# Kernel tuning notes

Measured on AMD Instinct MI355X. Metric: run time of the kernel, lower is better.

## Reference

```python
import jax, jax.numpy as jnp
import numpy as np

# Dims (match init_kwargs)
B, N, D_MODEL = 64, 64, 512
D_STATE = 512
D_ATT = D_MODEL
H, W, C, K = 128, 128, 16, 5
T = 32  # num_steps
HALF = K // 2


def _lin(key, out_d, in_d):
    kw, kb = jax.random.split(key)
    w = jax.random.normal(kw, (out_d, in_d), jnp.float32) * 0.02
    b = jax.random.normal(kb, (out_d,), jnp.float32) * 0.02
    return w, b


def setup_inputs() -> dict:
    key = jax.random.key(0)
    ks = jax.random.split(key, 12)
    token_reps = jax.random.normal(ks[0], (B, N, D_MODEL), jnp.float32)
    global_rep = jax.random.normal(ks[1], (B, D_MODEL), jnp.float32)
    attention_mask = jnp.ones((B, N), jnp.int32)
    w_init, b_init = _lin(ks[2], D_STATE, D_MODEL)
    wq, bq = _lin(ks[3], D_ATT, D_STATE)
    wk, bk = _lin(ks[4], D_ATT, D_MODEL)
    wv, bv = _lin(ks[5], D_ATT, D_MODEL)
    gru_in = D_ATT + D_MODEL
    w_ih, b_ih = _lin(ks[6], 3 * D_STATE, gru_in)
    w_hh, b_hh = _lin(ks[7], 3 * D_STATE, D_STATE)
    w_write, b_write = _lin(ks[8], C * K * K, D_STATE + D_ATT)
    w_loc, b_loc = _lin(ks[9], 3, D_STATE + D_ATT + D_MODEL)
    return dict(token_reps=token_reps, global_rep=global_rep, attention_mask=attention_mask,
                w_init=w_init, b_init=b_init, wq=wq, bq=bq, wk=wk, bk=bk, wv=wv, bv=bv,
                w_ih=w_ih, b_ih=b_ih, w_hh=w_hh, b_hh=b_hh,
                w_write=w_write, b_write=b_write, w_loc=w_loc, b_loc=b_loc)


def _forward(token_reps, global_rep, attention_mask,
             w_init, b_init, wq, bq, wk, bk, wv, bv,
             w_ih, b_ih, w_hh, b_hh, w_write, b_write, w_loc, b_loc):
    Bv = token_reps.shape[0]
    # Precompute keys/values (constant over steps)
    k_tok = token_reps @ wk.T + bk  # [B,N,d_att]
    v_tok = token_reps @ wv.T + bv  # [B,N,d_att]
    invalid = attention_mask == 0

    s0 = jnp.tanh(global_rep @ w_init.T + b_init)  # [B,d_state]
    # Padded canvas (NHWC): full KxK patches always fit; crop at the end
    # reproduces the torch clipped-window write exactly.
    canvas0 = jnp.zeros((Bv, H + 2 * HALF, W + 2 * HALF, C), jnp.float32)
    b_idx = jnp.arange(Bv)
    koff = jnp.arange(K)

    def step(carry, _):
        s, canvas_p = carry
        q = s @ wq.T + bq  # [B,d_att]
        scores = jnp.einsum('bd,bnd->bn', q, k_tok)
        scores = jnp.where(invalid, -1e9, scores)
        alpha = jax.nn.softmax(scores, axis=-1)
        r = jnp.einsum('bn,bnd->bd', alpha, v_tok)  # [B,d_att]
        # GRUCell (torch gate order r,z,n)
        x = jnp.concatenate([r, global_rep], axis=-1)
        gi = x @ w_ih.T + b_ih
        gh = s @ w_hh.T + b_hh
        ir, iz, inn = jnp.split(gi, 3, axis=-1)
        hr, hz, hn = jnp.split(gh, 3, axis=-1)
        rg = jax.nn.sigmoid(ir + hr)
        zg = jax.nn.sigmoid(iz + hz)
        ng = jnp.tanh(inn + rg * hn)
        s_new = (1.0 - zg) * ng + zg * s
        # Write patch
        patch = (jnp.concatenate([s_new, r], axis=-1) @ w_write.T + b_write)
        patch = patch.reshape(Bv, C, K, K).transpose(0, 2, 3, 1)  # [B,K,K,C]
        loc = jnp.concatenate([s_new, r, global_rep], axis=-1) @ w_loc.T + b_loc
        cx = jnp.tanh(loc[:, 0])
        cy = jnp.tanh(loc[:, 1])
        j = jnp.clip(jnp.round(0.5 * (cx + 1.0) * (W - 1)), 0, W - 1).astype(jnp.int32)
        i = jnp.clip(jnp.round(0.5 * (cy + 1.0) * (H - 1)), 0, H - 1).astype(jnp.int32)
        # padded coords: top-left of window in padded canvas is (i, j)
        rows = i[:, None] + koff  # [B,K]
        cols = j[:, None] + koff  # [B,K]
        canvas_p = canvas_p.at[b_idx[:, None, None], rows[:, :, None], cols[:, None, :]].add(patch)
        return (s_new, canvas_p), None

    (_, canvas_p), _ = jax.lax.scan(step, (s0, canvas0), None, length=T)
    canvas = canvas_p[:, HALF:HALF + H, HALF:HALF + W, :].transpose(0, 3, 1, 2)  # [B,C,H,W]
    return canvas


def reference(token_reps, global_rep, attention_mask,
              w_init, b_init, wq, bq, wk, bk, wv, bv,
              w_ih, b_ih, w_hh, b_hh, w_write, b_write, w_loc, b_loc):
    return _forward(token_reps, global_rep, attention_mask,
                    w_init, b_init, wq, bq, wk, bk, wv, bv,
                    w_ih, b_ih, w_hh, b_hh, w_write, b_write, w_loc, b_loc)
```

## Files before the change

### kernel.cpp

```cpp
#include <hip/hip_runtime.h>

#define BB 64
#define DD 512
#define TT 32

__device__ __forceinline__ float dot4(const float4 a, const float4 b) {
  return a.x * b.x + a.y * b.y + a.z * b.z + a.w * b.w;
}

__device__ __forceinline__ void cst(float* p, float v) {
  __hip_atomic_store(p, v, __ATOMIC_RELAXED, __HIP_MEMORY_SCOPE_AGENT);
}

__global__ void zero_k(float* __restrict__ out, int n4) {
  const int i = blockIdx.x * blockDim.x + threadIdx.x;
  if (i < n4) ((float4*)out)[i] = make_float4(0.f, 0.f, 0.f, 0.f);
}

__global__ void vecs_k(const float* __restrict__ wq, const float* __restrict__ bk,
                       const float* __restrict__ wk, const float* __restrict__ bq,
                       float* __restrict__ kqb, float* __restrict__ wkbq,
                       float* __restrict__ bqbk, unsigned* __restrict__ bar) {
  const int tid = threadIdx.x, bz = blockIdx.x;
  if (bz < 2) {
    const int d = bz * 256 + tid;
    float s = 0.f;
    for (int e = 0; e < DD; ++e) s += wq[e * DD + d] * bk[e];
    kqb[d] = s;
  } else {
    const int k = (bz - 2) * 256 + tid;
    float s = 0.f;
    for (int e = 0; e < DD; ++e) s += bq[e] * wk[e * DD + k];
    wkbq[k] = s;
    if (bz == 2 && tid == 0) {
      float t2 = 0.f;
      for (int e = 0; e < DD; ++e) t2 += bq[e] * bk[e];
      *bqbk = t2;
    }
    if (bz == 3) {
      if (tid < 16)
        __hip_atomic_store(bar + tid * 64, 0u, __ATOMIC_RELAXED, __HIP_MEMORY_SCOPE_AGENT);
      __hip_atomic_store(bar + 1024 + tid * 32, 0u, __ATOMIC_RELAXED, __HIP_MEMORY_SCOPE_AGENT);
    }
  }
}

__global__ __launch_bounds__(256) void gemm128_k(
    const float* __restrict__ A, int lda, int a_trans,
    const float* __restrict__ B, int ldb, int boff, int b_trans,
    const float* __restrict__ bias, float* __restrict__ C, long c_stride_z, int ldc,
    int kfrom, int klen, int act) {
  __shared__ __align__(16) float As[16][132];
  __shared__ __align__(16) float Bs[16][68];
  const int tid = threadIdx.x;
  const int tx = tid & 15, ty = tid >> 4;
  const int m0 = blockIdx.x * 128, n0 = blockIdx.y * 64;
  const int kbase = kfrom + blockIdx.z * klen;
  float* Ce = C + (long)blockIdx.z * c_stride_z;
  float acc[8][4];
#pragma unroll
  for (int i = 0; i < 8; ++i)
#pragma unroll
    for (int j = 0; j < 4; ++j) acc[i][j] = 0.f;

  for (int k0 = kbase; k0 < kbase + klen; k0 += 16) {
    if (!a_trans) {
      const int row = tid >> 1, half = tid & 1;
      const float* ap = A + (long)(m0 + row) * lda + k0 + half * 8;
      const float4 a0 = *(const float4*)ap;
      const float4 a1 = *(const float4*)(ap + 4);
      const int kb = half * 8;
      As[kb + 0][row] = a0.x; As[kb + 1][row] = a0.y; As[kb + 2][row] = a0.z; As[kb + 3][row] = a0.w;
      As[kb + 4][row] = a1.x; As[kb + 5][row] = a1.y; As[kb + 6][row] = a1.z; As[kb + 7][row] = a1.w;
    } else {
      const int kk = tid >> 4, mseg = tid & 15;
      const float* ap = A + (long)(k0 + kk) * lda + m0 + mseg * 8;
      *(float4*)&As[kk][mseg * 8] = *(const float4*)ap;
      *(float4*)&As[kk][mseg * 8 + 4] = *(const float4*)(ap + 4);
    }
    if (!b_trans) {
      const int n = tid >> 2, q = tid & 3;
      const float4 b0 = *(const float4*)(B + (long)(n0 + n) * ldb + boff + k0 + q * 4);
      Bs[q * 4 + 0][n] = b0.x; Bs[q * 4 + 1][n] = b0.y; Bs[q * 4 + 2][n] = b0.z; Bs[q * 4 + 3][n] = b0.w;
    } else {
      const int kk = tid >> 4, nq = tid & 15;
      *(float4*)&Bs[kk][nq * 4] = *(const float4*)(B + (long)(k0 + kk) * ldb + boff + n0 + nq * 4);
    }
    __syncthreads();
#pragma unroll
    for (int kk = 0; kk < 16; ++kk) {
      const float4 a0 = *(const float4*)&As[kk][ty * 8];
      const float4 a1 = *(const float4*)&As[kk][ty * 8 + 4];
      const float4 b0 = *(const float4*)&Bs[kk][tx * 4];
      const float am[8] = {a0.x, a0.y, a0.z, a0.w, a1.x, a1.y, a1.z, a1.w};
#pragma unroll
      for (int i = 0; i < 8; ++i) {
        acc[i][0] += am[i] * b0.x; acc[i][1] += am[i] * b0.y;
        acc[i][2] += am[i] * b0.z; acc[i][3] += am[i] * b0.w;
      }
    }
    __syncthreads();
  }
  float4 bv = make_float4(0.f, 0.f, 0.f, 0.f);
  if (bias) bv = *(const float4*)(bias + n0 + tx * 4);
#pragma unroll
  for (int i = 0; i < 8; ++i) {
    const int m = m0 + ty * 8 + i;
    float4 v = make_float4(acc[i][0] + bv.x, acc[i][1] + bv.y, acc[i][2] + bv.z, acc[i][3] + bv.w);
    if (act == 1) { v.x = tanhf(v.x); v.y = tanhf(v.y); v.z = tanhf(v.z); v.w = tanhf(v.w); }
    *(float4*)&Ce[(long)m * ldc + n0 + tx * 4] = v;
  }
}

__global__ __launch_bounds__(256) void gemm128_dual_k(
    const float* __restrict__ A,
    const float* __restrict__ B0, const float* __restrict__ bias0, float* __restrict__ C0,
    const float* __restrict__ B1, const float* __restrict__ bias1, float* __restrict__ C1) {
  __shared__ __align__(16) float As[16][132];
  __shared__ __align__(16) float Bs[16][68];
  const int tid = threadIdx.x;
  const int tx = tid & 15, ty = tid >> 4;
  const int m0 = blockIdx.x * 128, n0 = blockIdx.y * 64;
  const float* B = blockIdx.z ? B1 : B0;
  const float* bias = blockIdx.z ? bias1 : bias0;
  float* C = blockIdx.z ? C1 : C0;
  float acc[8][4];
#pragma unroll
  for (int i = 0; i < 8; ++i)
#pragma unroll
    for (int j = 0; j < 4; ++j) acc[i][j] = 0.f;

  for (int k0 = 0; k0 < 512; k0 += 16) {
    {
      const int row = tid >> 1, half = tid & 1;
      const float* ap = A + (long)(m0 + row) * 512 + k0 + half * 8;
      const float4 a0 = *(const float4*)ap;
      const float4 a1 = *(const float4*)(ap + 4);
      const int kb = half * 8;
      As[kb + 0][row] = a0.x; As[kb + 1][row] = a0.y; As[kb + 2][row] = a0.z; As[kb + 3][row] = a0.w;
      As[kb + 4][row] = a1.x; As[kb + 5][row] = a1.y; As[kb + 6][row] = a1.z; As[kb + 7][row] = a1.w;
    }
    {
      const int n = tid >> 2, q = tid & 3;
      const float4 b0 = *(const float4*)(B + (long)(n0 + n) * 512 + k0 + q * 4);
      Bs[q * 4 + 0][n] = b0.x; Bs[q * 4 + 1][n] = b0.y; Bs[q * 4 + 2][n] = b0.z; Bs[q * 4 + 3][n] = b0.w;
    }
    __syncthreads();
#pragma unroll
    for (int kk = 0; kk < 16; ++kk) {
      const float4 a0 = *(const float4*)&As[kk][ty * 8];
      const float4 a1 = *(const float4*)&As[kk][ty * 8 + 4];
      const float4 b0 = *(const float4*)&Bs[kk][tx * 4];
      const float am[8] = {a0.x, a0.y, a0.z, a0.w, a1.x, a1.y, a1.z, a1.w};
#pragma unroll
      for (int i = 0; i < 8; ++i) {
        acc[i][0] += am[i] * b0.x; acc[i][1] += am[i] * b0.y;
        acc[i][2] += am[i] * b0.z; acc[i][3] += am[i] * b0.w;
      }
    }
    __syncthreads();
  }
  const float4 bvv = *(const float4*)(bias + n0 + tx * 4);
#pragma unroll
  for (int i = 0; i < 8; ++i) {
    const int m = m0 + ty * 8 + i;
    float4 v = make_float4(acc[i][0] + bvv.x, acc[i][1] + bvv.y, acc[i][2] + bvv.z, acc[i][3] + bvv.w);
    *(float4*)&C[(long)m * 512 + n0 + tx * 4] = v;
  }
}

__global__ void combine4_k(const float* __restrict__ p, float* __restrict__ out) {
  const int i = blockIdx.x * blockDim.x + threadIdx.x;
  const float4 a = ((const float4*)p)[i];
  const float4 b = ((const float4*)p)[i + 65536];
  const float4 c = ((const float4*)p)[i + 131072];
  const float4 d = ((const float4*)p)[i + 196608];
  ((float4*)out)[i] = make_float4(a.x + b.x + c.x + d.x, a.y + b.y + c.y + d.y,
                                  a.z + b.z + c.z + d.z, a.w + b.w + c.w + d.w);
}

__global__ __launch_bounds__(256) void gemm_k(
    const float* __restrict__ A, int lda, int a_trans,
    const float* __restrict__ B, int ldb, int boff, int b_trans,
    const float* __restrict__ bias,
    float* __restrict__ C, int ldc, int M, int N, int K, int act) {
  __shared__ __align__(16) float As2[32][68];
  __shared__ __align__(16) float Bs2[32][68];
  const int tid = threadIdx.x;
  const int tx = tid & 15, ty = tid >> 4;
  const int m0 = blockIdx.x * 64, n0 = blockIdx.y * 64;
  float acc[4][4] = {};
  for (int k0 = 0; k0 < K; k0 += 32) {
    {
      const int r = tid >> 2, cg2 = (tid & 3) * 8;
      const float* ap = A + (long)(m0 + r) * lda + k0 + cg2;
      const float4 a0 = *(const float4*)ap;
      const float4 a1 = *(const float4*)(ap + 4);
      As2[cg2 + 0][r] = a0.x; As2[cg2 + 1][r] = a0.y; As2[cg2 + 2][r] = a0.z; As2[cg2 + 3][r] = a0.w;
      As2[cg2 + 4][r] = a1.x; As2[cg2 + 5][r] = a1.y; As2[cg2 + 6][r] = a1.z; As2[cg2 + 7][r] = a1.w;
    }
    {
      const int r = tid >> 2, cg2 = (tid & 3) * 8;
      float4 b0 = make_float4(0.f, 0.f, 0.f, 0.f);
      float4 b1 = make_float4(0.f, 0.f, 0.f, 0.f);
      if (n0 + r < N) {
        const float* bp = B + (long)(n0 + r) * ldb + boff + k0 + cg2;
        b0 = *(const float4*)bp;
        b1 = *(const float4*)(bp + 4);
      }
      Bs2[cg2 + 0][r] = b0.x; Bs2[cg2 + 1][r] = b0.y; Bs2[cg2 + 2][r] = b0.z; Bs2[cg2 + 3][r] = b0.w;
      Bs2[cg2 + 4][r] = b1.x; Bs2[cg2 + 5][r] = b1.y; Bs2[cg2 + 6][r] = b1.z; Bs2[cg2 + 7][r] = b1.w;
    }
    __syncthreads();
#pragma unroll
    for (int kk = 0; kk < 32; ++kk) {
      const float4 av = *(const float4*)&As2[kk][ty * 4];
      const float4 bv = *(const float4*)&Bs2[kk][tx * 4];
      acc[0][0] += av.x * bv.x; acc[0][1] += av.x * bv.y; acc[0][2] += av.x * bv.z; acc[0][3] += av.x * bv.w;
      acc[1][0] += av.y * bv.x; acc[1][1] += av.y * bv.y; acc[1][2] += av.y * bv.z; acc[1][3] += av.y * bv.w;
      acc[2][0] += av.z * bv.x; acc[2][1] += av.z * bv.y; acc[2][2] += av.z * bv.z; acc[2][3] += av.z * bv.w;
      acc[3][0] += av.w * bv.x; acc[3][1] += av.w * bv.y; acc[3][2] += av.w * bv.z; acc[3][3] += av.w * bv.w;
    }
    __syncthreads();
  }
#pragma unroll
  for (int i = 0; i < 4; ++i) {
    const int m = m0 + ty * 4 + i;
#pragma unroll
    for (int j = 0; j < 4; ++j) {
      const int n = n0 + tx * 4 + j;
      if (n < N) {
        float v = acc[i][j] + (bias ? bias[n] : 0.f);
        if (act == 1) v = tanhf(v);
        C[(long)m * ldc + n] = v;
      }
    }
  }
}

__device__ __forceinline__ void grid_barrier(unsigned* __restrict__ bar, unsigned gen) {
  __syncthreads();
  const int blk = blockIdx.x, tid = threadIdx.x;
  unsigned* gctr = bar;
  unsigned* rel = bar + 1024;
  if (blk == 0) {
    if (tid == 0)
      __hip_atomic_fetch_add(gctr, 1u, __ATOMIC_RELAXED, __HIP_MEMORY_SCOPE_AGENT);
    if (tid < 16) {
      while (__hip_atomic_load(gctr + tid * 64, __ATOMIC_RELAXED, __HIP_MEMORY_SCOPE_AGENT) < gen * 16u)
        __builtin_amdgcn_s_sleep(1);
    }
    __syncthreads();
    __hip_atomic_store(rel + tid * 32, gen, __ATOMIC_RELAXED, __HIP_MEMORY_SCOPE_AGENT);
  } else {
    if (tid == 0) {
      __hip_atomic_fetch_add(gctr + (blk >> 4) * 64, 1u, __ATOMIC_RELAXED, __HIP_MEMORY_SCOPE_AGENT);
      while (__hip_atomic_load(rel + blk * 32, __ATOMIC_RELAXED, __HIP_MEMORY_SCOPE_AGENT) < gen)
        __builtin_amdgcn_s_sleep(1);
    }
  }
  __syncthreads();
}

__global__ __launch_bounds__(256, 1) void loop_k(
    const float* __restrict__ ktil, const float* __restrict__ cbn,
    const float* __restrict__ vt, const float* __restrict__ locg,
    float* __restrict__ sbuf, float* __restrict__ rbuf,
    const float* __restrict__ w_write, const float* __restrict__ b_write,
    const float* __restrict__ w_loc, const int* __restrict__ amask,
    float* __restrict__ canvas, const float* __restrict__ gig,
    const float* __restrict__ w_ih, const float* __restrict__ w_hh,
    const float* __restrict__ b_hh, unsigned* __restrict__ bar) {
  __shared__ __align__(16) float smem[10048];
  __shared__ __align__(16) float wpl[12288];
  float* sm_act = smem;
  float* sm_val = smem + 9216;
  float* sm_sc  = smem + 9408;
  float* sm_s   = smem;
  float* sm_r   = smem + 4608;
  float* sm_g   = smem + 9216;

  const int blk = blockIdx.x, tid = threadIdx.x, lane = tid & 63;
  const bool is_attn = (blk < 64);
  const bool is_patch = (blk >= 64) && (blk < 224);
  unsigned nsync = 0;

  int p_rg = 0, p_bg = 0;
  if (is_patch) {
    const int g = blk - 64;
    p_bg = g & 3; p_rg = g >> 2;
    for (int idx = tid; idx < 3072; idx += 256) {
      const int rho = idx >> 8, f4 = idx & 255;
      const int col = f4 << 2;
      const int cc = col >> 5, jj = (col >> 2) & 7;
      const int dcol = (cc << 5) | ((jj ^ (cc & 7)) << 2);
      const float* src = (rho < 10) ? (w_write + (long)(p_rg * 10 + rho) * 1024 + col)
                                    : (w_loc + (long)(rho - 10) * 1536 + col);
      *(float4*)(wpl + rho * 1024 + dcol) = *(const float4*)src;
    }
  }

  float4 wg[3][8];
  const int g_dg = blk & 63, g_bg = blk >> 6;
  {
    const int c = tid & 15, sl = tid >> 4;
#pragma unroll
    for (int i = 0; i < 3; ++i) {
      const int rho = sl * 3 + i;
      const float* wsrc;
      if (rho < 24) {
        const int g2 = rho >> 3, di = rho & 7;
        wsrc = w_ih + (long)(g2 * 512 + g_dg * 8 + di) * 1024 + c * 32;
      } else {
        const int rh = rho - 24, g2 = rh >> 3, di = rh & 7;
        wsrc = w_hh + (long)(g2 * 512 + g_dg * 8 + di) * 512 + c * 32;
      }
#pragma unroll
      for (int j = 0; j < 8; ++j) wg[i][j] = *(const float4*)(wsrc + 4 * j);
    }
  }
  __syncthreads();

  for (int t = 0; t <= TT; ++t) {
    const float* s_cur = sbuf + (long)t * (BB * DD);
    float* r_cur = rbuf + (long)t * (BB * DD);
    const float* r_prev = r_cur - BB * DD;

    if (is_attn) {
      if (t < TT) {
        const int b = blk, wrp = tid >> 6;
        const float* sb = s_cur + (long)b * DD;
        const float4 sva = *(const float4*)(sb + lane * 8);
        const float4 svb = *(const float4*)(sb + lane * 8 + 4);
        for (int h8 = 0; h8 < 2; ++h8) {
          const float* kbase = ktil + ((long)(b * 64 + wrp * 16 + h8 * 8)) * DD + lane * 8;
          float4 ka[8], kb2[8];
#pragma unroll
          for (int i = 0; i < 8; ++i) {
            ka[i] = *(const float4*)(kbase + (long)i * DD);
            kb2[i] = *(const float4*)(kbase + (long)i * DD + 4);
          }
#pragma unroll
          for (int i = 0; i < 8; ++i) {
            float p = dot4(ka[i], sva) + dot4(kb2[i], svb);
#pragma unroll
            for (int off = 32; off; off >>= 1) p += __shfl_xor(p, off);
            if (lane == 0) {
              const int n = wrp * 16 + h8 * 8 + i;
              float sc = p + cbn[b * 64 + n];
              if (amask[b * 64 + n] == 0) sc = -1e9f;
              sm_sc[n] = sc;
            }
          }
        }
        __syncthreads();
        if (tid < 64) {
          const float v = sm_sc[tid];
          float m = v;
#pragma unroll
          for (int off = 32; off; off >>= 1) m = fmaxf(m, __shfl_xor(m, off));
          const float e = expf(v - m);
          float l2 = e;
#pragma unroll
          for (int off = 32; off; off >>= 1) l2 += __shfl_xor(l2, off);
          sm_sc[tid] = e / l2;
        }
        __syncthreads();
        float rx = 0.f, ry = 0.f;
        const float* vb = vt + (long)b * 64 * DD + (tid << 1);
        for (int n0 = 0; n0 < 64; n0 += 8) {
          float2 vv[8];
#pragma unroll
          for (int i = 0; i < 8; ++i)
            vv[i] = *(const float2*)(vb + (long)(n0 + i) * DD);
#pragma unroll
          for (int i = 0; i < 8; ++i) {
            const float a = sm_sc[n0 + i];
            rx = fmaf(a, vv[i].x, rx);
            ry = fmaf(a, vv[i].y, ry);
          }
        }
        cst(r_cur + b * DD + (tid << 1), rx);
        cst(r_cur + b * DD + (tid << 1) + 1, ry);
      }
    } else if (is_patch) {
      if (t >= 1) {
        const int c = tid & 31, sl = tid >> 5;
        const int tr = sl & 3, bgsub = sl >> 2;
        for (int h = 0; h < 2; ++h) {
          __syncthreads();
          {
            const int b_i8 = tid >> 5, l = tid & 31;
            const int b = p_bg * 16 + h * 8 + b_i8;
            const float* sp = s_cur + (long)b * DD + l * 16;
            const float* rp = r_prev + (long)b * DD + l * 16;
            float* dsd = sm_act + b_i8 * 1152 + (l >> 1) * 36 + (l & 1) * 16;
            float* drd = sm_act + b_i8 * 1152 + (16 + (l >> 1)) * 36 + (l & 1) * 16;
#pragma unroll
            for (int jj = 0; jj < 4; ++jj) {
              *(float4*)(dsd + 4 * jj) = *(const float4*)(sp + 4 * jj);
              *(float4*)(drd + 4 * jj) = *(const float4*)(rp + 4 * jj);
            }
          }
          __syncthreads();
          float4 wreg[3][8];
#pragma unroll
          for (int i = 0; i < 3; ++i) {
            const float* wrow = wpl + (tr * 3 + i) * 1024 + (c << 5);
#pragma unroll
            for (int j = 0; j < 8; ++j)
              wreg[i][j] = *(const float4*)(wrow + ((j ^ (c & 7)) << 2));
          }
          for (int bi = 0; bi < 4; ++bi) {
            const int bl = bgsub * 4 + bi;
            const int babs = p_bg * 16 + h * 8 + bl;
            const float* ap = sm_act + bl * 1152 + c * 36;
            float a0 = 0.f, a1 = 0.f, a2 = 0.f;
#pragma unroll
            for (int j = 0; j < 8; ++j) {
              const float4 av = *(const float4*)(ap + 4 * j);
              a0 += dot4(wreg[0][j], av);
              a1 += dot4(wreg[1][j], av);
              a2 += dot4(wreg[2][j], av);
            }
#pragma unroll
            for (int m = 1; m < 32; m <<= 1) {
              a0 += __shfl_xor(a0, m);
              a1 += __shfl_xor(a1, m);
              a2 += __shfl_xor(a2, m);
            }
            if (c == 0) {
              const int bslot = h * 8 + bl;
              const float av3[3] = {a0, a1, a2};
#pragma unroll
              for (int i = 0; i < 3; ++i) {
                const int rho = tr * 3 + i;
                float v = av3[i];
                if (rho >= 10) v += locg[babs * 2 + (rho - 10)];
                sm_val[rho * 16 + bslot] = v;
              }
            }
          }
        }
        __syncthreads();
        if (tid < 160) {
          const int ri = tid >> 4, bl2 = tid & 15;
          const int row = p_rg * 10 + ri;
          const int b = p_bg * 16 + bl2;
          const float val = sm_val[ri * 16 + bl2] + b_write[row];
          const float lx = sm_val[10 * 16 + bl2];
          const float ly = sm_val[11 * 16 + bl2];
          const int jx = min(127, max(0, (int)rintf(0.5f * (tanhf(lx) + 1.f) * 127.f)));
          const int iy = min(127, max(0, (int)rintf(0.5f * (tanhf(ly) + 1.f) * 127.f)));
          const int cc = row / 25, rem = row % 25, ki = rem / 5, kj = rem % 5;
          const int y = iy + ki - 2, x = jx + kj - 2;
          if (y >= 0 && y < 128 && x >= 0 && x < 128)
            atomicAdd(canvas + ((((long)b * 16 + cc) * 128 + y) * 128 + x), val);
        }
      }
    }

    if (t == TT) break;

    grid_barrier(bar, ++nsync);

    {
      float* s_nxt = sbuf + (long)(t + 1) * (BB * DD);
      const int c = tid & 15, sl = tid >> 4;
      for (int h = 0; h < 2; ++h) {
        __syncthreads();
        {
          const int b_i8 = tid >> 5, l = tid & 31;
          const int b = g_bg * 16 + h * 8 + b_i8;
          const float* sp = s_cur + (long)b * DD + l * 16;
          const float* rp = r_cur + (long)b * DD + l * 16;
          float* dsd = sm_s + b_i8 * 576 + (l >> 1) * 36 + (l & 1) * 16;
          float* drd = sm_r + b_i8 * 576 + (l >> 1) * 36 + (l & 1) * 16;
#pragma unroll
          for (int jj = 0; jj < 4; ++jj) {
            *(float4*)(dsd + 4 * jj) = *(const float4*)(sp + 4 * jj);
            *(float4*)(drd + 4 * jj) = *(const float4*)(rp + 4 * jj);
          }
        }
        __syncthreads();
        const float* base = (sl < 8) ? sm_r : sm_s;
        for (int bl = 0; bl < 8; ++bl) {
          const float* ap = base + bl * 576 + c * 36;
          float a0 = 0.f, a1 = 0.f, a2 = 0.f;
#pragma unroll
          for (int j = 0; j < 8; ++j) {
            const float4 av = *(const float4*)(ap + 4 * j);
            a0 += dot4(wg[0][j], av);
            a1 += dot4(wg[1][j], av);
            a2 += dot4(wg[2][j], av);
          }
#pragma unroll
          for (int m = 1; m < 16; m <<= 1) {
            a0 += __shfl_xor(a0, m);
            a1 += __shfl_xor(a1, m);
            a2 += __shfl_xor(a2, m);
          }
          if (c == 0) {
            const int bslot = h * 8 + bl;
            sm_g[bslot * 52 + sl * 3 + 0] = a0;
            sm_g[bslot * 52 + sl * 3 + 1] = a1;
            sm_g[bslot * 52 + sl * 3 + 2] = a2;
          }
        }
      }
      __syncthreads();
      if (tid < 128) {
        const int b_i = tid >> 3, di = tid & 7;
        const int b = g_bg * 16 + b_i, d = g_dg * 8 + di;
        const float ir = sm_g[b_i * 52 + di]        + gig[b * 1536 + d];
        const float iz = sm_g[b_i * 52 + 8 + di]    + gig[b * 1536 + 512 + d];
        const float in = sm_g[b_i * 52 + 16 + di]   + gig[b * 1536 + 1024 + d];
        const float hr = sm_g[b_i * 52 + 24 + di]   + b_hh[d];
        const float hz = sm_g[b_i * 52 + 32 + di]   + b_hh[512 + d];
        const float hn = sm_g[b_i * 52 + 40 + di]   + b_hh[1024 + d];
        const float rg2 = 1.f / (1.f + expf(-(ir + hr)));
        const float zg = 1.f / (1.f + expf(-(iz + hz)));
        const float ng = tanhf(in + rg2 * hn);
        const float sprev = s_cur[(long)b * DD + d];
        cst(s_nxt + (long)b * DD + d, (1.f - zg) * ng + zg * sprev);
      }
    }

    grid_barrier(bar, ++nsync);
  }
}

extern "C" void kernel_launch(void* const* d_in, const int* in_sizes, int n_in,
                              void* d_out, int out_size, void* d_ws, size_t ws_size,
                              hipStream_t stream) {
  const float* tok     = (const float*)d_in[0];
  const float* grep    = (const float*)d_in[1];
  const int*   amask   = (const int*)d_in[2];
  const float* w_init  = (const float*)d_in[3];
  const float* b_init  = (const float*)d_in[4];
  const float* wq      = (const float*)d_in[5];
  const float* bq      = (const float*)d_in[6];
  const float* wk      = (const float*)d_in[7];
  const float* bk      = (const float*)d_in[8];
  const float* wv      = (const float*)d_in[9];
  const float* bv      = (const float*)d_in[10];
  const float* w_ih    = (const float*)d_in[11];
  const float* b_ih    = (const float*)d_in[12];
  const float* w_hh    = (const float*)d_in[13];
  const float* b_hh    = (const float*)d_in[14];
  const float* w_write = (const float*)d_in[15];
  const float* b_write = (const float*)d_in[16];
  const float* w_loc   = (const float*)d_in[17];
  const float* b_loc   = (const float*)d_in[18];
  float* canvas = (float*)d_out;

  float* ws = (float*)d_ws;
  float* ktil = ws;
  float* vtw  = ktil + 2097152;
  float* Aqk  = vtw + 2097152;
  float* gig  = Aqk + 262144;
  float* cbn  = gig + 98304;
  float* sbuf = cbn + 4096;
  float* rbuf = sbuf + 1081344;
  float* locg = rbuf + 1048576;
  float* kqb  = locg + 128;
  float* wkbq = kqb + 512;
  float* bqbk = wkbq + 512;
  unsigned* bar = (unsigned*)(bqbk + 64);

  zero_k<<<16384, 256, 0, stream>>>(canvas, 16777216 / 4);
  vecs_k<<<4, 256, 0, stream>>>(wq, bk, wk, bq, kqb, wkbq, bqbk, bar);
  gemm128_k<<<dim3(4, 8, 4), 256, 0, stream>>>(wq, 512, 1, wk, 512, 0, 1,
                                               nullptr, vtw, 262144L, 512, 0, 128, 0);
  combine4_k<<<256, 256, 0, stream>>>(vtw, Aqk);
  gemm128_dual_k<<<dim3(32, 8, 2), 256, 0, stream>>>(tok, Aqk, kqb, ktil, wv, bv, vtw);
  gemm_k<<<dim3(64, 1), 256, 0, stream>>>(tok, 512, 0, wkbq, 0, 0, 0, bqbk, cbn, 1, 4096, 1, 512, 0);
  gemm_k<<<dim3(1, 24), 256, 0, stream>>>(grep, 512, 0, w_ih, 1024, 512, 0, b_ih, gig, 1536, 64, 1536, 512, 0);
  gemm_k<<<dim3(1, 8), 256, 0, stream>>>(grep, 512, 0, w_init, 512, 0, 0, b_init, sbuf, 512, 64, 512, 512, 1);
  gemm_k<<<dim3(1, 1), 256, 0, stream>>>(grep, 512, 0, w_loc, 1536, 1024, 0, b_loc, locg, 2, 64, 2, 512, 0);

  loop_k<<<256, 256, 0, stream>>>(ktil, cbn, vtw, locg, sbuf, rbuf, w_write, b_write,
                                  w_loc, amask, canvas, gig, w_ih, w_hh, b_hh, bar);
}
```

Measured before the change: 1.134 ms.

## Decouple patch blocks from grid barrier and defer canvas writes to separate kernel

```diff
diff --git a/kernel.cpp b/kernel.cpp
--- a/kernel.cpp
+++ b/kernel.cpp
@@ -10,11 +10,6 @@
 
 __device__ __forceinline__ void cst(float* p, float v) {
   __hip_atomic_store(p, v, __ATOMIC_RELAXED, __HIP_MEMORY_SCOPE_AGENT);
-}
-
-__global__ void zero_k(float* __restrict__ out, int n4) {
-  const int i = blockIdx.x * blockDim.x + threadIdx.x;
-  if (i < n4) ((float4*)out)[i] = make_float4(0.f, 0.f, 0.f, 0.f);
 }
 
 __global__ void vecs_k(const float* __restrict__ wq, const float* __restrict__ bk,
@@ -238,7 +233,7 @@
   }
 }
 
-__device__ __forceinline__ void grid_barrier(unsigned* __restrict__ bar, unsigned gen) {
+__device__ __forceinline__ void ag_barrier(unsigned* __restrict__ bar, unsigned gen) {
   __syncthreads();
   const int blk = blockIdx.x, tid = threadIdx.x;
   unsigned* gctr = bar;
@@ -246,12 +241,13 @@
   if (blk == 0) {
     if (tid == 0)
       __hip_atomic_fetch_add(gctr, 1u, __ATOMIC_RELAXED, __HIP_MEMORY_SCOPE_AGENT);
-    if (tid < 16) {
+    if (tid < 4) {
       while (__hip_atomic_load(gctr + tid * 64, __ATOMIC_RELAXED, __HIP_MEMORY_SCOPE_AGENT) < gen * 16u)
         __builtin_amdgcn_s_sleep(1);
     }
     __syncthreads();
-    __hip_atomic_store(rel + tid * 32, gen, __ATOMIC_RELAXED, __HIP_MEMORY_SCOPE_AGENT);
+    if (tid < 224)
+      __hip_atomic_store(rel + tid * 32, gen, __ATOMIC_RELAXED, __HIP_MEMORY_SCOPE_AGENT);
   } else {
     if (tid == 0) {
       __hip_atomic_fetch_add(gctr + (blk >> 4) * 64, 1u, __ATOMIC_RELAXED, __HIP_MEMORY_SCOPE_AGENT);
@@ -268,214 +264,51 @@
     float* __restrict__ sbuf, float* __restrict__ rbuf,
     const float* __restrict__ w_write, const float* __restrict__ b_write,
     const float* __restrict__ w_loc, const int* __restrict__ amask,
-    float* __restrict__ canvas, const float* __restrict__ gig,
-    const float* __restrict__ w_ih, const float* __restrict__ w_hh,
-    const float* __restrict__ b_hh, unsigned* __restrict__ bar) {
-  __shared__ __align__(16) float smem[10048];
-  __shared__ __align__(16) float wpl[12288];
-  float* sm_act = smem;
-  float* sm_val = smem + 9216;
-  float* sm_sc  = smem + 9408;
-  float* sm_s   = smem;
-  float* sm_r   = smem + 4608;
-  float* sm_g   = smem + 9216;
-
+    float* __restrict__ patchbuf, float* __restrict__ locbuf,
+    const float* __restrict__ gig, const float* __restrict__ w_ih,
+    const float* __restrict__ w_hh, const float* __restrict__ b_hh,
+    unsigned* __restrict__ bar) {
+  __shared__ __align__(16) float smem[38272];
   const int blk = blockIdx.x, tid = threadIdx.x, lane = tid & 63;
-  const bool is_attn = (blk < 64);
-  const bool is_patch = (blk >= 64) && (blk < 224);
-  unsigned nsync = 0;
-
-  int p_rg = 0, p_bg = 0;
-  if (is_patch) {
+  unsigned* rel = bar + 1024;
+
+  if (blk >= 64) {
+    float* wpl    = smem;
+    float* sm_act = smem + 12288;
+    float* sm_val = smem + 21504;
     const int g = blk - 64;
-    p_bg = g & 3; p_rg = g >> 2;
+    const int p_bg = g & 3, p_rg = g >> 2;
     for (int idx = tid; idx < 3072; idx += 256) {
       const int rho = idx >> 8, f4 = idx & 255;
       const int col = f4 << 2;
-      const int cc = col >> 5, jj = (col >> 2) & 7;
-      const int dcol = (cc << 5) | ((jj ^ (cc & 7)) << 2);
+      const int cc2 = col >> 5, jj = (col >> 2) & 7;
+      const int dcol = (cc2 << 5) | ((jj ^ (cc2 & 7)) << 2);
       const float* src = (rho < 10) ? (w_write + (long)(p_rg * 10 + rho) * 1024 + col)
                                     : (w_loc + (long)(rho - 10) * 1536 + col);
       *(float4*)(wpl + rho * 1024 + dcol) = *(const float4*)src;
     }
-  }
-
-  float4 wg[3][8];
-  const int g_dg = blk & 63, g_bg = blk >> 6;
-  {
-    const int c = tid & 15, sl = tid >> 4;
-#pragma unroll
-    for (int i = 0; i < 3; ++i) {
-      const int rho = sl * 3 + i;
-      const float* wsrc;
-      if (rho < 24) {
-        const int g2 = rho >> 3, di = rho & 7;
-        wsrc = w_ih + (long)(g2 * 512 + g_dg * 8 + di) * 1024 + c * 32;
-      } else {
-        const int rh = rho - 24, g2 = rh >> 3, di = rh & 7;
-        wsrc = w_hh + (long)(g2 * 512 + g_dg * 8 + di) * 512 + c * 32;
-      }
-#pragma unroll
-      for (int j = 0; j < 8; ++j) wg[i][j] = *(const float4*)(wsrc + 4 * j);
-    }
-  }
-  __syncthreads();
-
-  for (int t = 0; t <= TT; ++t) {
-    const float* s_cur = sbuf + (long)t * (BB * DD);
-    float* r_cur = rbuf + (long)t * (BB * DD);
-    const float* r_prev = r_cur - BB * DD;
-
-    if (is_attn) {
-      if (t < TT) {
-        const int b = blk, wrp = tid >> 6;
-        const float* sb = s_cur + (long)b * DD;
-        const float4 sva = *(const float4*)(sb + lane * 8);
-        const float4 svb = *(const float4*)(sb + lane * 8 + 4);
-        for (int h8 = 0; h8 < 2; ++h8) {
-          const float* kbase = ktil + ((long)(b * 64 + wrp * 16 + h8 * 8)) * DD + lane * 8;
-          float4 ka[8], kb2[8];
-#pragma unroll
-          for (int i = 0; i < 8; ++i) {
-            ka[i] = *(const float4*)(kbase + (long)i * DD);
-            kb2[i] = *(const float4*)(kbase + (long)i * DD + 4);
-          }
-#pragma unroll
-          for (int i = 0; i < 8; ++i) {
-            float p = dot4(ka[i], sva) + dot4(kb2[i], svb);
-#pragma unroll
-            for (int off = 32; off; off >>= 1) p += __shfl_xor(p, off);
-            if (lane == 0) {
-              const int n = wrp * 16 + h8 * 8 + i;
-              float sc = p + cbn[b * 64 + n];
-              if (amask[b * 64 + n] == 0) sc = -1e9f;
-              sm_sc[n] = sc;
-            }
-          }
-        }
-        __syncthreads();
-        if (tid < 64) {
-          const float v = sm_sc[tid];
-          float m = v;
-#pragma unroll
-          for (int off = 32; off; off >>= 1) m = fmaxf(m, __shfl_xor(m, off));
-          const float e = expf(v - m);
-          float l2 = e;
-#pragma unroll
-          for (int off = 32; off; off >>= 1) l2 += __shfl_xor(l2, off);
-          sm_sc[tid] = e / l2;
-        }
-        __syncthreads();
-        float rx = 0.f, ry = 0.f;
-        const float* vb = vt + (long)b * 64 * DD + (tid << 1);
-        for (int n0 = 0; n0 < 64; n0 += 8) {
-          float2 vv[8];
-#pragma unroll
-          for (int i = 0; i < 8; ++i)
-            vv[i] = *(const float2*)(vb + (long)(n0 + i) * DD);
-#pragma unroll
-          for (int i = 0; i < 8; ++i) {
-            const float a = sm_sc[n0 + i];
-            rx = fmaf(a, vv[i].x, rx);
-            ry = fmaf(a, vv[i].y, ry);
-          }
-        }
-        cst(r_cur + b * DD + (tid << 1), rx);
-        cst(r_cur + b * DD + (tid << 1) + 1, ry);
-      }
-    } else if (is_patch) {
-      if (t >= 1) {
-        const int c = tid & 31, sl = tid >> 5;
-        const int tr = sl & 3, bgsub = sl >> 2;
-        for (int h = 0; h < 2; ++h) {
-          __syncthreads();
-          {
-            const int b_i8 = tid >> 5, l = tid & 31;
-            const int b = p_bg * 16 + h * 8 + b_i8;
-            const float* sp = s_cur + (long)b * DD + l * 16;
-            const float* rp = r_prev + (long)b * DD + l * 16;
-            float* dsd = sm_act + b_i8 * 1152 + (l >> 1) * 36 + (l & 1) * 16;
-            float* drd = sm_act + b_i8 * 1152 + (16 + (l >> 1)) * 36 + (l & 1) * 16;
-#pragma unroll
-            for (int jj = 0; jj < 4; ++jj) {
-              *(float4*)(dsd + 4 * jj) = *(const float4*)(sp + 4 * jj);
-              *(float4*)(drd + 4 * jj) = *(const float4*)(rp + 4 * jj);
-            }
-          }
-          __syncthreads();
-          float4 wreg[3][8];
-#pragma unroll
-          for (int i = 0; i < 3; ++i) {
-            const float* wrow = wpl + (tr * 3 + i) * 1024 + (c << 5);
-#pragma unroll
-            for (int j = 0; j < 8; ++j)
-              wreg[i][j] = *(const float4*)(wrow + ((j ^ (c & 7)) << 2));
-          }
-          for (int bi = 0; bi < 4; ++bi) {
-            const int bl = bgsub * 4 + bi;
-            const int babs = p_bg * 16 + h * 8 + bl;
-            const float* ap = sm_act + bl * 1152 + c * 36;
-            float a0 = 0.f, a1 = 0.f, a2 = 0.f;
-#pragma unroll
-            for (int j = 0; j < 8; ++j) {
-              const float4 av = *(const float4*)(ap + 4 * j);
-              a0 += dot4(wreg[0][j], av);
-              a1 += dot4(wreg[1][j], av);
-              a2 += dot4(wreg[2][j], av);
-            }
-#pragma unroll
-            for (int m = 1; m < 32; m <<= 1) {
-              a0 += __shfl_xor(a0, m);
-              a1 += __shfl_xor(a1, m);
-              a2 += __shfl_xor(a2, m);
-            }
-            if (c == 0) {
-              const int bslot = h * 8 + bl;
-              const float av3[3] = {a0, a1, a2};
-#pragma unroll
-              for (int i = 0; i < 3; ++i) {
-                const int rho = tr * 3 + i;
-                float v = av3[i];
-                if (rho >= 10) v += locg[babs * 2 + (rho - 10)];
-                sm_val[rho * 16 + bslot] = v;
-              }
-            }
-          }
-        }
-        __syncthreads();
-        if (tid < 160) {
-          const int ri = tid >> 4, bl2 = tid & 15;
-          const int row = p_rg * 10 + ri;
-          const int b = p_bg * 16 + bl2;
-          const float val = sm_val[ri * 16 + bl2] + b_write[row];
-          const float lx = sm_val[10 * 16 + bl2];
-          const float ly = sm_val[11 * 16 + bl2];
-          const int jx = min(127, max(0, (int)rintf(0.5f * (tanhf(lx) + 1.f) * 127.f)));
-          const int iy = min(127, max(0, (int)rintf(0.5f * (tanhf(ly) + 1.f) * 127.f)));
-          const int cc = row / 25, rem = row % 25, ki = rem / 5, kj = rem % 5;
-          const int y = iy + ki - 2, x = jx + kj - 2;
-          if (y >= 0 && y < 128 && x >= 0 && x < 128)
-            atomicAdd(canvas + ((((long)b * 16 + cc) * 128 + y) * 128 + x), val);
-        }
-      }
-    }
-
-    if (t == TT) break;
-
-    grid_barrier(bar, ++nsync);
-
-    {
-      float* s_nxt = sbuf + (long)(t + 1) * (BB * DD);
-      const int c = tid & 15, sl = tid >> 4;
+    __syncthreads();
+
+    const int c = tid & 31, sl = tid >> 5;
+    const int tr = sl & 3, bgsub = sl >> 2;
+    for (int t = 1; t <= TT; ++t) {
+      if (tid == 0) {
+        while (__hip_atomic_load(rel + blk * 32, __ATOMIC_RELAXED, __HIP_MEMORY_SCOPE_AGENT) < 2u * (unsigned)t)
+          __builtin_amdgcn_s_sleep(2);
+      }
+      __syncthreads();
+      const float* s_cur = sbuf + (long)t * (BB * DD);
+      const float* r_prev = rbuf + (long)(t - 1) * (BB * DD);
+
       for (int h = 0; h < 2; ++h) {
         __syncthreads();
         {
           const int b_i8 = tid >> 5, l = tid & 31;
-          const int b = g_bg * 16 + h * 8 + b_i8;
+          const int b = p_bg * 16 + h * 8 + b_i8;
           const float* sp = s_cur + (long)b * DD + l * 16;
-          const float* rp = r_cur + (long)b * DD + l * 16;
-          float* dsd = sm_s + b_i8 * 576 + (l >> 1) * 36 + (l & 1) * 16;
-          float* drd = sm_r + b_i8 * 576 + (l >> 1) * 36 + (l & 1) * 16;
+          const float* rp = r_prev + (long)b * DD + l * 16;
+          float* dsd = sm_act + b_i8 * 1152 + (l >> 1) * 36 + (l & 1) * 16;
+          float* drd = sm_act + b_i8 * 1152 + (16 + (l >> 1)) * 36 + (l & 1) * 16;
 #pragma unroll
           for (int jj = 0; jj < 4; ++jj) {
             *(float4*)(dsd + 4 * jj) = *(const float4*)(sp + 4 * jj);
@@ -483,51 +316,250 @@
           }
         }
         __syncthreads();
-        const float* base = (sl < 8) ? sm_r : sm_s;
-        for (int bl = 0; bl < 8; ++bl) {
-          const float* ap = base + bl * 576 + c * 36;
+        float4 wreg[3][8];
+#pragma unroll
+        for (int i = 0; i < 3; ++i) {
+          const float* wrow = wpl + (tr * 3 + i) * 1024 + (c << 5);
+#pragma unroll
+          for (int j = 0; j < 8; ++j)
+            wreg[i][j] = *(const float4*)(wrow + ((j ^ (c & 7)) << 2));
+        }
+        for (int bi = 0; bi < 4; ++bi) {
+          const int bl = bgsub * 4 + bi;
+          const int babs = p_bg * 16 + h * 8 + bl;
+          const float* ap = sm_act + bl * 1152 + c * 36;
           float a0 = 0.f, a1 = 0.f, a2 = 0.f;
 #pragma unroll
           for (int j = 0; j < 8; ++j) {
             const float4 av = *(const float4*)(ap + 4 * j);
-            a0 += dot4(wg[0][j], av);
-            a1 += dot4(wg[1][j], av);
-            a2 += dot4(wg[2][j], av);
+            a0 += dot4(wreg[0][j], av);
+            a1 += dot4(wreg[1][j], av);
+            a2 += dot4(wreg[2][j], av);
           }
 #pragma unroll
-          for (int m = 1; m < 16; m <<= 1) {
+          for (int m = 1; m < 32; m <<= 1) {
             a0 += __shfl_xor(a0, m);
             a1 += __shfl_xor(a1, m);
             a2 += __shfl_xor(a2, m);
           }
           if (c == 0) {
             const int bslot = h * 8 + bl;
-            sm_g[bslot * 52 + sl * 3 + 0] = a0;
-            sm_g[bslot * 52 + sl * 3 + 1] = a1;
-            sm_g[bslot * 52 + sl * 3 + 2] = a2;
+            const float av3[3] = {a0, a1, a2};
+#pragma unroll
+            for (int i = 0; i < 3; ++i) {
+              const int rho = tr * 3 + i;
+              float v = av3[i];
+              if (rho >= 10) v += locg[babs * 2 + (rho - 10)];
+              sm_val[rho * 16 + bslot] = v;
+            }
           }
         }
       }
       __syncthreads();
-      if (tid < 128) {
-        const int b_i = tid >> 3, di = tid & 7;
-        const int b = g_bg * 16 + b_i, d = g_dg * 8 + di;
-        const float ir = sm_g[b_i * 52 + di]        + gig[b * 1536 + d];
-        const float iz = sm_g[b_i * 52 + 8 + di]    + gig[b * 1536 + 512 + d];
-        const float in = sm_g[b_i * 52 + 16 + di]   + gig[b * 1536 + 1024 + d];
-        const float hr = sm_g[b_i * 52 + 24 + di]   + b_hh[d];
-        const float hz = sm_g[b_i * 52 + 32 + di]   + b_hh[512 + d];
-        const float hn = sm_g[b_i * 52 + 40 + di]   + b_hh[1024 + d];
-        const float rg2 = 1.f / (1.f + expf(-(ir + hr)));
-        const float zg = 1.f / (1.f + expf(-(iz + hz)));
-        const float ng = tanhf(in + rg2 * hn);
-        const float sprev = s_cur[(long)b * DD + d];
-        cst(s_nxt + (long)b * DD + d, (1.f - zg) * ng + zg * sprev);
-      }
-    }
-
-    grid_barrier(bar, ++nsync);
-  }
+      const int u = t - 1;
+      if (tid < 160) {
+        const int ri = tid >> 4, bl2 = tid & 15;
+        const int row = p_rg * 10 + ri;
+        const int b = p_bg * 16 + bl2;
+        patchbuf[((long)u * 64 + b) * 400 + row] = sm_val[ri * 16 + bl2] + b_write[row];
+      }
+      if (p_rg == 0 && tid < 16) {
+        const int b = p_bg * 16 + tid;
+        const float lx = sm_val[160 + tid];
+        const float ly = sm_val[176 + tid];
+        const int jx = min(127, max(0, (int)rintf(0.5f * (tanhf(lx) + 1.f) * 127.f)));
+        const int iy = min(127, max(0, (int)rintf(0.5f * (tanhf(ly) + 1.f) * 127.f)));
+        locbuf[((long)u * 64 + b) * 2] = (float)jx;
+        locbuf[((long)u * 64 + b) * 2 + 1] = (float)iy;
+      }
+    }
+    return;
+  }
+
+  float* vlds  = smem;
+  float* sm_s4 = smem + 32768;
+  float* sm_r4 = smem + 35072;
+  float* sm_g  = smem + 37376;
+  float* sm_sc = smem + 38208;
+  const int b = blk;
+
+  for (int i = tid; i < 8192; i += 256)
+    ((float4*)vlds)[i] = ((const float4*)(vt + (long)b * 32768))[i];
+
+  float4 wg[3][8];
+  {
+    const int c = tid & 15, sl = tid >> 4;
+#pragma unroll
+    for (int i = 0; i < 3; ++i) {
+      const int rho = sl * 3 + i;
+      const float* wsrc;
+      if (rho < 24) {
+        const int g2 = rho >> 3, di = rho & 7;
+        wsrc = w_ih + (long)(g2 * 512 + blk * 8 + di) * 1024 + c * 32;
+      } else {
+        const int rh = rho - 24, g2 = rh >> 3, di = rh & 7;
+        wsrc = w_hh + (long)(g2 * 512 + blk * 8 + di) * 512 + c * 32;
+      }
+#pragma unroll
+      for (int j = 0; j < 8; ++j) wg[i][j] = *(const float4*)(wsrc + 4 * j);
+    }
+  }
+  __syncthreads();
+
+  unsigned gen = 0;
+  for (int t = 0; t < TT; ++t) {
+    const float* s_cur = sbuf + (long)t * (BB * DD);
+    float* r_cur = rbuf + (long)t * (BB * DD);
+
+    {
+      const int wrp = tid >> 6;
+      const float* sb = s_cur + (long)b * DD;
+      const float4 sva = *(const float4*)(sb + lane * 8);
+      const float4 svb = *(const float4*)(sb + lane * 8 + 4);
+      for (int h8 = 0; h8 < 2; ++h8) {
+        const float* kbase = ktil + ((long)(b * 64 + wrp * 16 + h8 * 8)) * DD + lane * 8;
+        float4 ka[8], kb2[8];
+#pragma unroll
+        for (int i = 0; i < 8; ++i) {
+          ka[i] = *(const float4*)(kbase + (long)i * DD);
+          kb2[i] = *(const float4*)(kbase + (long)i * DD + 4);
+        }
+#pragma unroll
+        for (int i = 0; i < 8; ++i) {
+          float p = dot4(ka[i], sva) + dot4(kb2[i], svb);
+#pragma unroll
+          for (int off = 32; off; off >>= 1) p += __shfl_xor(p, off);
+          if (lane == 0) {
+            const int n = wrp * 16 + h8 * 8 + i;
+            float sc = p + cbn[b * 64 + n];
+            if (amask[b * 64 + n] == 0) sc = -1e9f;
+            sm_sc[n] = sc;
+          }
+        }
+      }
+      __syncthreads();
+      if (tid < 64) {
+        const float v = sm_sc[tid];
+        float m = v;
+#pragma unroll
+        for (int off = 32; off; off >>= 1) m = fmaxf(m, __shfl_xor(m, off));
+        const float e = expf(v - m);
+        float l2 = e;
+#pragma unroll
+        for (int off = 32; off; off >>= 1) l2 += __shfl_xor(l2, off);
+        sm_sc[tid] = e / l2;
+      }
+      __syncthreads();
+      float rx = 0.f, ry = 0.f;
+      const float* vb2 = vlds + (tid << 1);
+      for (int n0 = 0; n0 < 64; n0 += 8) {
+        float2 vv[8];
+#pragma unroll
+        for (int i = 0; i < 8; ++i)
+          vv[i] = *(const float2*)(vb2 + (n0 + i) * 512);
+#pragma unroll
+        for (int i = 0; i < 8; ++i) {
+          const float a = sm_sc[n0 + i];
+          rx = fmaf(a, vv[i].x, rx);
+          ry = fmaf(a, vv[i].y, ry);
+        }
+      }
+      cst(r_cur + (long)b * DD + (tid << 1), rx);
+      cst(r_cur + (long)b * DD + (tid << 1) + 1, ry);
+    }
+
+    ag_barrier(bar, ++gen);
+
+    {
+      float* s_nxt = sbuf + (long)(t + 1) * (BB * DD);
+      const int c = tid & 15, sl = tid >> 4;
+      for (int q = 0; q < 4; ++q) {
+        for (int h = 0; h < 4; ++h) {
+          __syncthreads();
+          {
+            const int bb = tid >> 6, l = tid & 63;
+            const int bidx = q * 16 + h * 4 + bb;
+            const float* sp = s_cur + (long)bidx * DD + l * 8;
+            const float* rp = r_cur + (long)bidx * DD + l * 8;
+            float* dsd = sm_s4 + bb * 576 + (l >> 2) * 36 + (l & 3) * 8;
+            float* drd = sm_r4 + bb * 576 + (l >> 2) * 36 + (l & 3) * 8;
+            *(float4*)dsd = *(const float4*)sp;
+            *(float4*)(dsd + 4) = *(const float4*)(sp + 4);
+            *(float4*)drd = *(const float4*)rp;
+            *(float4*)(drd + 4) = *(const float4*)(rp + 4);
+          }
+          __syncthreads();
+          const float* base = (sl < 8) ? sm_r4 : sm_s4;
+          for (int bl = 0; bl < 4; ++bl) {
+            const float* ap = base + bl * 576 + c * 36;
+            float a0 = 0.f, a1 = 0.f, a2 = 0.f;
+#pragma unroll
+            for (int j = 0; j < 8; ++j) {
+              const float4 av = *(const float4*)(ap + 4 * j);
+              a0 += dot4(wg[0][j], av);
+              a1 += dot4(wg[1][j], av);
+              a2 += dot4(wg[2][j], av);
+            }
+#pragma unroll
+            for (int m = 1; m < 16; m <<= 1) {
+              a0 += __shfl_xor(a0, m);
+              a1 += __shfl_xor(a1, m);
+              a2 += __shfl_xor(a2, m);
+            }
+            if (c == 0) {
+              const int bslot = h * 4 + bl;
+              sm_g[bslot * 52 + sl * 3 + 0] = a0;
+              sm_g[bslot * 52 + sl * 3 + 1] = a1;
+              sm_g[bslot * 52 + sl * 3 + 2] = a2;
+            }
+          }
+        }
+        __syncthreads();
+        if (tid < 128) {
+          const int b_i = tid >> 3, di = tid & 7;
+          const int bb2 = q * 16 + b_i, d = blk * 8 + di;
+          const float ir = sm_g[b_i * 52 + di]      + gig[bb2 * 1536 + d];
+          const float iz = sm_g[b_i * 52 + 8 + di]  + gig[bb2 * 1536 + 512 + d];
+          const float in = sm_g[b_i * 52 + 16 + di] + gig[bb2 * 1536 + 1024 + d];
+          const float hr = sm_g[b_i * 52 + 24 + di] + b_hh[d];
+          const float hz = sm_g[b_i * 52 + 32 + di] + b_hh[512 + d];
+          const float hn = sm_g[b_i * 52 + 40 + di] + b_hh[1024 + d];
+          const float rg2 = 1.f / (1.f + expf(-(ir + hr)));
+          const float zg = 1.f / (1.f + expf(-(iz + hz)));
+          const float ng = tanhf(in + rg2 * hn);
+          const float sprev = s_cur[(long)bb2 * DD + d];
+          cst(s_nxt + (long)bb2 * DD + d, (1.f - zg) * ng + zg * sprev);
+        }
+      }
+    }
+
+    ag_barrier(bar, ++gen);
+  }
+}
+
+__global__ __launch_bounds__(256) void canvas_k(const float* __restrict__ pb,
+                                                const float* __restrict__ lb,
+                                                float* __restrict__ canvas) {
+  __shared__ float ch[16384];
+  const int blk = blockIdx.x, tid = threadIdx.x;
+  const int b = blk >> 4, c = blk & 15;
+  for (int i = tid; i < 4096; i += 256)
+    ((float4*)ch)[i] = make_float4(0.f, 0.f, 0.f, 0.f);
+  __syncthreads();
+  for (int u = 0; u < TT; ++u) {
+    const int jx = (int)lb[((long)u * 64 + b) * 2];
+    const int iy = (int)lb[((long)u * 64 + b) * 2 + 1];
+    if (tid < 25) {
+      const float v = pb[((long)u * 64 + b) * 400 + c * 25 + tid];
+      const int ki = tid / 5, kj = tid % 5;
+      const int y = iy + ki - 2, x = jx + kj - 2;
+      if (y >= 0 && y < 128 && x >= 0 && x < 128) ch[y * 128 + x] += v;
+    }
+    __syncthreads();
+  }
+  float* dst = canvas + ((long)b * 16 + c) * 16384;
+  for (int i = tid; i < 4096; i += 256)
+    ((float4*)dst)[i] = ((float4*)ch)[i];
 }
 
 extern "C" void kernel_launch(void* const* d_in, const int* in_sizes, int n_in,
@@ -567,8 +599,9 @@
   float* wkbq = kqb + 512;
   float* bqbk = wkbq + 512;
   unsigned* bar = (unsigned*)(bqbk + 64);
-
-  zero_k<<<16384, 256, 0, stream>>>(canvas, 16777216 / 4);
+  float* patchbuf = (float*)(bar + 16384);
+  float* locbuf = patchbuf + 819200;
+
   vecs_k<<<4, 256, 0, stream>>>(wq, bk, wk, bq, kqb, wkbq, bqbk, bar);
   gemm128_k<<<dim3(4, 8, 4), 256, 0, stream>>>(wq, 512, 1, wk, 512, 0, 1,
                                                nullptr, vtw, 262144L, 512, 0, 128, 0);
@@ -579,6 +612,7 @@
   gemm_k<<<dim3(1, 8), 256, 0, stream>>>(grep, 512, 0, w_init, 512, 0, 0, b_init, sbuf, 512, 64, 512, 512, 1);
   gemm_k<<<dim3(1, 1), 256, 0, stream>>>(grep, 512, 0, w_loc, 1536, 1024, 0, b_loc, locg, 2, 64, 2, 512, 0);
 
-  loop_k<<<256, 256, 0, stream>>>(ktil, cbn, vtw, locg, sbuf, rbuf, w_write, b_write,
-                                  w_loc, amask, canvas, gig, w_ih, w_hh, b_hh, bar);
-}
+  loop_k<<<224, 256, 0, stream>>>(ktil, cbn, vtw, locg, sbuf, rbuf, w_write, b_write,
+                                  w_loc, amask, patchbuf, locbuf, gig, w_ih, w_hh, b_hh, bar);
+  canvas_k<<<1024, 256, 0, stream>>>(patchbuf, locbuf, canvas);
+}
```

After: 2.034 ms. +79.4%, slower.

## Defer canvas scatter to a separate LDS-accumulating kernel, drop zero fill

Applied to the files above, without the earlier changes.

```diff
diff --git a/kernel.cpp b/kernel.cpp
--- a/kernel.cpp
+++ b/kernel.cpp
@@ -10,11 +10,6 @@
 
 __device__ __forceinline__ void cst(float* p, float v) {
   __hip_atomic_store(p, v, __ATOMIC_RELAXED, __HIP_MEMORY_SCOPE_AGENT);
-}
-
-__global__ void zero_k(float* __restrict__ out, int n4) {
-  const int i = blockIdx.x * blockDim.x + threadIdx.x;
-  if (i < n4) ((float4*)out)[i] = make_float4(0.f, 0.f, 0.f, 0.f);
 }
 
 __global__ void vecs_k(const float* __restrict__ wq, const float* __restrict__ bk,
@@ -268,9 +263,10 @@
     float* __restrict__ sbuf, float* __restrict__ rbuf,
     const float* __restrict__ w_write, const float* __restrict__ b_write,
     const float* __restrict__ w_loc, const int* __restrict__ amask,
-    float* __restrict__ canvas, const float* __restrict__ gig,
-    const float* __restrict__ w_ih, const float* __restrict__ w_hh,
-    const float* __restrict__ b_hh, unsigned* __restrict__ bar) {
+    float* __restrict__ patchbuf, float* __restrict__ locbuf,
+    const float* __restrict__ gig, const float* __restrict__ w_ih,
+    const float* __restrict__ w_hh, const float* __restrict__ b_hh,
+    unsigned* __restrict__ bar) {
   __shared__ __align__(16) float smem[10048];
   __shared__ __align__(16) float wpl[12288];
   float* sm_act = smem;
@@ -292,8 +288,8 @@
     for (int idx = tid; idx < 3072; idx += 256) {
       const int rho = idx >> 8, f4 = idx & 255;
       const int col = f4 << 2;
-      const int cc = col >> 5, jj = (col >> 2) & 7;
-      const int dcol = (cc << 5) | ((jj ^ (cc & 7)) << 2);
+      const int cc2 = col >> 5, jj = (col >> 2) & 7;
+      const int dcol = (cc2 << 5) | ((jj ^ (cc2 & 7)) << 2);
       const float* src = (rho < 10) ? (w_write + (long)(p_rg * 10 + rho) * 1024 + col)
                                     : (w_loc + (long)(rho - 10) * 1536 + col);
       *(float4*)(wpl + rho * 1024 + dcol) = *(const float4*)src;
@@ -380,8 +376,8 @@
             ry = fmaf(a, vv[i].y, ry);
           }
         }
-        cst(r_cur + b * DD + (tid << 1), rx);
-        cst(r_cur + b * DD + (tid << 1) + 1, ry);
+        cst(r_cur + (long)b * DD + (tid << 1), rx);
+        cst(r_cur + (long)b * DD + (tid << 1) + 1, ry);
       }
     } else if (is_patch) {
       if (t >= 1) {
@@ -443,19 +439,21 @@
           }
         }
         __syncthreads();
+        const int u = t - 1;
         if (tid < 160) {
           const int ri = tid >> 4, bl2 = tid & 15;
           const int row = p_rg * 10 + ri;
           const int b = p_bg * 16 + bl2;
-          const float val = sm_val[ri * 16 + bl2] + b_write[row];
-          const float lx = sm_val[10 * 16 + bl2];
-          const float ly = sm_val[11 * 16 + bl2];
+          patchbuf[((long)u * 64 + b) * 400 + row] = sm_val[ri * 16 + bl2] + b_write[row];
+        }
+        if (p_rg == 0 && tid < 16) {
+          const int b = p_bg * 16 + tid;
+          const float lx = sm_val[160 + tid];
+          const float ly = sm_val[176 + tid];
           const int jx = min(127, max(0, (int)rintf(0.5f * (tanhf(lx) + 1.f) * 127.f)));
           const int iy = min(127, max(0, (int)rintf(0.5f * (tanhf(ly) + 1.f) * 127.f)));
-          const int cc = row / 25, rem = row % 25, ki = rem / 5, kj = rem % 5;
-          const int y = iy + ki - 2, x = jx + kj - 2;
-          if (y >= 0 && y < 128 && x >= 0 && x < 128)
-            atomicAdd(canvas + ((((long)b * 16 + cc) * 128 + y) * 128 + x), val);
+          locbuf[((long)u * 64 + b) * 2] = (float)jx;
+          locbuf[((long)u * 64 + b) * 2 + 1] = (float)iy;
         }
       }
     }
@@ -528,6 +526,31 @@
 
     grid_barrier(bar, ++nsync);
   }
+}
+
+__global__ __launch_bounds__(256) void canvas_k(const float* __restrict__ pb,
+                                                const float* __restrict__ lb,
+                                                float* __restrict__ canvas) {
+  __shared__ float ch[16384];
+  const int blk = blockIdx.x, tid = threadIdx.x;
+  const int b = blk >> 4, c = blk & 15;
+  for (int i = tid; i < 4096; i += 256)
+    ((float4*)ch)[i] = make_float4(0.f, 0.f, 0.f, 0.f);
+  __syncthreads();
+  for (int u = 0; u < TT; ++u) {
+    const int jx = (int)lb[((long)u * 64 + b) * 2];
+    const int iy = (int)lb[((long)u * 64 + b) * 2 + 1];
+    if (tid < 25) {
+      const float v = pb[((long)u * 64 + b) * 400 + c * 25 + tid];
+      const int ki = tid / 5, kj = tid % 5;
+      const int y = iy + ki - 2, x = jx + kj - 2;
+      if (y >= 0 && y < 128 && x >= 0 && x < 128) ch[y * 128 + x] += v;
+    }
+    __syncthreads();
+  }
+  float* dst = canvas + ((long)b * 16 + c) * 16384;
+  for (int i = tid; i < 4096; i += 256)
+    ((float4*)dst)[i] = ((float4*)ch)[i];
 }
 
 extern "C" void kernel_launch(void* const* d_in, const int* in_sizes, int n_in,
@@ -567,8 +590,9 @@
   float* wkbq = kqb + 512;
   float* bqbk = wkbq + 512;
   unsigned* bar = (unsigned*)(bqbk + 64);
-
-  zero_k<<<16384, 256, 0, stream>>>(canvas, 16777216 / 4);
+  float* patchbuf = (float*)(bar + 16384);
+  float* locbuf = patchbuf + 819200;
+
   vecs_k<<<4, 256, 0, stream>>>(wq, bk, wk, bq, kqb, wkbq, bqbk, bar);
   gemm128_k<<<dim3(4, 8, 4), 256, 0, stream>>>(wq, 512, 1, wk, 512, 0, 1,
                                                nullptr, vtw, 262144L, 512, 0, 128, 0);
@@ -580,5 +604,6 @@
   gemm_k<<<dim3(1, 1), 256, 0, stream>>>(grep, 512, 0, w_loc, 1536, 1024, 0, b_loc, locg, 2, 64, 2, 512, 0);
 
   loop_k<<<256, 256, 0, stream>>>(ktil, cbn, vtw, locg, sbuf, rbuf, w_write, b_write,
-                                  w_loc, amask, canvas, gig, w_ih, w_hh, b_hh, bar);
-}
+                                  w_loc, amask, patchbuf, locbuf, gig, w_ih, w_hh, b_hh, bar);
+  canvas_k<<<1024, 256, 0, stream>>>(patchbuf, locbuf, canvas);
+}
```

Measured after the change: 1.158 ms. 1.02x slower.
